# Optimization experiments

Measured on AMD Instinct MI355X. Metric: run time of the kernel, lower is better.

The kernel has to match this reference:

```python
import jax, jax.numpy as jnp
import numpy as np

B, C, Q, D = 64, 512, 64, 256  # D = 2 * hidden_size; similarity weight has 3*D = 768 entries


def _length_mask(key, batch, seqlen):
    # realistic padding masks: each row has a random valid prefix length in [seqlen//2, seqlen]
    lens = jax.random.randint(key, (batch,), seqlen // 2, seqlen + 1)
    return (jnp.arange(seqlen)[None, :] < lens[:, None]).astype(jnp.int32)


def setup_inputs() -> dict:
    key = jax.random.key(0)
    k1, k2, k3, k4, k5 = jax.random.split(key, 5)
    context = jax.random.normal(k1, (B, C, D), dtype=jnp.float32)
    question = jax.random.normal(k2, (B, Q, D), dtype=jnp.float32)
    context_mask = _length_mask(k3, B, C)
    question_mask = _length_mask(k4, B, Q)
    w = jax.random.normal(k5, (3 * D,), dtype=jnp.float32) * (1.0 / np.sqrt(3 * D))
    return {"context": context, "question": question,
            "context_mask": context_mask, "question_mask": question_mask, "w": w}


def reference(context, question, context_mask, question_mask, w):
    d = context.shape[-1]
    # Linear([c, q, c*q]) with no bias decomposes exactly into three terms.
    w_c, w_q, w_m = w[:d], w[d:2 * d], w[2 * d:]
    sim = ((context @ w_c)[:, :, None]                      # [B, C, 1]
           + (question @ w_q)[:, None, :]                   # [B, 1, Q]
           + jnp.einsum('bcd,bqd->bcq', context * w_m, question))  # [B, C, Q]
    neg = jnp.finfo(sim.dtype).min
    # context-to-query attention (mask question positions)
    sim_q = jnp.where(question_mask[:, None, :] != 0, sim, neg)
    a = jax.nn.softmax(sim_q, axis=2)                        # [B, C, Q]
    c2q = jnp.einsum('bcq,bqd->bcd', a, question)            # [B, C, D]
    # query-to-context attention (max over Q, mask context positions)
    sim_max = jnp.max(sim, axis=2)                           # [B, C]
    sim_max = jnp.where(context_mask != 0, sim_max, neg)
    b = jax.nn.softmax(sim_max, axis=1)                      # [B, C]
    q2c = jnp.einsum('bc,bcd->bd', b, context)[:, None, :]   # [B, 1, D]
    q2c = jnp.broadcast_to(q2c, context.shape)               # [B, C, D]
    g = jnp.concatenate([context, c2q, context * c2q, context * q2c], axis=-1)
    return g
```

## Files before the change

### kernel.cpp

```cpp
#include <hip/hip_runtime.h>
#include <hip/hip_bf16.h>
#include <float.h>

#define B_ 64
#define C_ 512
#define Q_ 64
#define D_ 256

typedef _Float16 f16x8 __attribute__((ext_vector_type(8)));
typedef float f32x4 __attribute__((ext_vector_type(4)));

union U4H8 { uint4 u; f16x8 h; };
union UH2 { _Float16 h[2]; uint32_t u; };

__device__ __forceinline__ uint32_t packh2(float a, float b) {
  UH2 v; v.h[0] = (_Float16)a; v.h[1] = (_Float16)b; return v.u;
}

__device__ __forceinline__ float wred_sum(float v) {
#pragma unroll
  for (int off = 32; off > 0; off >>= 1) v += __shfl_xor(v, off, 64);
  return v;
}
__device__ __forceinline__ float wred_max(float v) {
#pragma unroll
  for (int off = 32; off > 0; off >>= 1) v = fmaxf(v, __shfl_xor(v, off, 64));
  return v;
}

__global__ __launch_bounds__(256) void k_rowdot(const float* __restrict__ src,
                                                const float* __restrict__ wgt,
                                                float* __restrict__ out, int nrows) {
  int wv = threadIdx.x >> 6, ln = threadIdx.x & 63;
  int row = blockIdx.x * 4 + wv;
  if (row >= nrows) return;
  float4 s4 = *(const float4*)(src + (size_t)row * D_ + 4 * ln);
  float4 w4 = *(const float4*)(wgt + 4 * ln);
  float p = s4.x * w4.x + s4.y * w4.y + s4.z * w4.z + s4.w * w4.w;
  p = wred_sum(p);
  if (ln == 0) out[row] = p;
}

__global__ __launch_bounds__(256) void k_prepack(const float* __restrict__ qst,
                                                 const float* __restrict__ w,
                                                 uint32_t* __restrict__ qraw_img,
                                                 uint32_t* __restrict__ qT_img,
                                                 float* __restrict__ qwq) {
  const int b = blockIdx.x;
  const int sub = blockIdx.y;
  const int t = threadIdx.x;
  const float* qb = qst + (size_t)b * Q_ * D_;
#pragma unroll
  for (int it = 0; it < 8; ++it) {
    int idx = sub * 2048 + it * 256 + t;
    int q = idx >> 7, jp = idx & 127;
    float2 v = *(const float2*)(qb + q * D_ + 2 * jp);
    int ch = jp >> 2;
    int phys = (ch & ~7) | ((ch & 7) ^ (q & 7));
    qraw_img[(size_t)b * 8192 + q * 128 + phys * 4 + (jp & 3)] = packh2(v.x, v.y);
  }
  {
    int d = sub * 64 + (t >> 2);
    uint32_t* dst = qT_img + (size_t)b * 8192 + d * 32;
#pragma unroll
    for (int k = 0; k < 2; ++k) {
      int qc = (t & 3) * 2 + k;
      uint32_t tmp[4];
#pragma unroll
      for (int e = 0; e < 4; ++e) {
        int q0 = qc * 8 + e * 2;
        tmp[e] = packh2(qb[q0 * D_ + d], qb[(q0 + 1) * D_ + d]);
      }
      int pc = qc ^ (d & 7);
      *(uint4*)(dst + pc * 4) = uint4{tmp[0], tmp[1], tmp[2], tmp[3]};
    }
  }
  if (sub == 0) {
    int q = t >> 2, sl = t & 3;
    float p = 0.f;
#pragma unroll
    for (int i = 0; i < 16; ++i) {
      float4 v = *(const float4*)(qb + q * D_ + sl * 64 + i * 4);
      float4 ww = *(const float4*)(w + D_ + sl * 64 + i * 4);
      p += v.x * ww.x + v.y * ww.y + v.z * ww.z + v.w * ww.w;
    }
    p += __shfl_xor(p, 1, 64);
    p += __shfl_xor(p, 2, 64);
    if (sl == 0) qwq[b * Q_ + q] = p;
  }
}

template<int IMG>
__global__ __launch_bounds__(256, 2) void k_main(
    const float* __restrict__ ctx, const float* __restrict__ qst,
    const int* __restrict__ qmask, const float* __restrict__ w,
    const float* __restrict__ qwq_g,
    const uint32_t* __restrict__ qraw_img, const uint32_t* __restrict__ qT_img,
    float* __restrict__ g, float* __restrict__ simmax_g) {
  __shared__ __align__(16) ushort qraw[Q_ * D_];
  __shared__ __align__(16) ushort qT[D_ * Q_];
  __shared__ __align__(16) ushort pbuf[4][16 * Q_];
  __shared__ float qwq_l[Q_];
  __shared__ int   qml_l[Q_];

  const int bid = blockIdx.x;
  const int b = bid & 63;
  const int c0 = (bid >> 6) * 64;
  const int t = threadIdx.x;
  const int wv = t >> 6, ln = t & 63;
  const int lc = ln & 15;
  const int lg = ln >> 4;
  const int c0w = c0 + wv * 16;

  if constexpr (IMG) {
    const uint32_t* qr_src = qraw_img + (size_t)b * 8192;
    const uint32_t* qt_src = qT_img + (size_t)b * 8192;
#pragma unroll
    for (int i = 0; i < 8; ++i)
      __builtin_amdgcn_global_load_lds(
          (const __attribute__((address_space(1))) uint32_t*)(qr_src + i * 1024 + t * 4),
          (__attribute__((address_space(3))) uint32_t*)((uint32_t*)qraw + i * 1024 + t * 4),
          16, 0, 0);
#pragma unroll
    for (int i = 0; i < 8; ++i)
      __builtin_amdgcn_global_load_lds(
          (const __attribute__((address_space(1))) uint32_t*)(qt_src + i * 1024 + t * 4),
          (__attribute__((address_space(3))) uint32_t*)((uint32_t*)qT + i * 1024 + t * 4),
          16, 0, 0);
  }

  f16x8 bfrag[8];
  float cwc_p = 0.f;
  const float* crow = ctx + ((size_t)b * C_ + c0w + lc) * D_;
  float* grow0 = g + ((size_t)b * C_ + c0w + lc) * (4 * D_);
#pragma unroll
  for (int kk = 0; kk < 8; ++kk) {
    int kb = kk * 32 + lg * 8;
    float4 cv0 = *(const float4*)(crow + kb);
    float4 cv1 = *(const float4*)(crow + kb + 4);
    float4 wc0 = *(const float4*)(w + kb);
    float4 wc1 = *(const float4*)(w + kb + 4);
    float4 wm0 = *(const float4*)(w + 2 * D_ + kb);
    float4 wm1 = *(const float4*)(w + 2 * D_ + kb + 4);
    cwc_p += cv0.x * wc0.x + cv0.y * wc0.y + cv0.z * wc0.z + cv0.w * wc0.w
           + cv1.x * wc1.x + cv1.y * wc1.y + cv1.z * wc1.z + cv1.w * wc1.w;
    bfrag[kk][0] = (_Float16)(cv0.x * wm0.x);
    bfrag[kk][1] = (_Float16)(cv0.y * wm0.y);
    bfrag[kk][2] = (_Float16)(cv0.z * wm0.z);
    bfrag[kk][3] = (_Float16)(cv0.w * wm0.w);
    bfrag[kk][4] = (_Float16)(cv1.x * wm1.x);
    bfrag[kk][5] = (_Float16)(cv1.y * wm1.y);
    bfrag[kk][6] = (_Float16)(cv1.z * wm1.z);
    bfrag[kk][7] = (_Float16)(cv1.w * wm1.w);
    *(float4*)(grow0 + kb) = cv0;
    *(float4*)(grow0 + kb + 4) = cv1;
  }
  float cwc = cwc_p;
  cwc += __shfl_xor(cwc, 16, 64);
  cwc += __shfl_xor(cwc, 32, 64);

  if constexpr (!IMG) {
    const float* qb = qst + (size_t)b * Q_ * D_;
#pragma unroll 4
    for (int it = 0; it < 32; ++it) {
      int idx = it * 256 + t;
      int q = idx >> 7, jp = idx & 127;
      float2 v = *(const float2*)(qb + q * D_ + 2 * jp);
      int ch = jp >> 2;
      int phys = (ch & ~7) | ((ch & 7) ^ (q & 7));
      *(uint32_t*)((char*)qraw + q * 512 + phys * 16 + (jp & 3) * 4) = packh2(v.x, v.y);
    }
#pragma unroll 4
    for (int it = 0; it < 32; ++it) {
      int q = t & 63;
      int jp = (t >> 6) + 4 * it;
      float2 v = *(const float2*)(qb + q * D_ + 2 * jp);
      int d0 = 2 * jp, d1 = d0 + 1;
      UH2 h0; h0.h[0] = (_Float16)v.x;
      UH2 h1; h1.h[0] = (_Float16)v.y;
      *(ushort*)((char*)qT + d0 * 128 + (((q >> 3) ^ (d0 & 7)) << 4) + (q & 7) * 2) = (ushort)(h0.u & 0xffff);
      *(ushort*)((char*)qT + d1 * 128 + (((q >> 3) ^ (d1 & 7)) << 4) + (q & 7) * 2) = (ushort)(h1.u & 0xffff);
    }
  }
  if (t < Q_) { qwq_l[t] = qwq_g[b * Q_ + t]; qml_l[t] = qmask[b * Q_ + t]; }
  __syncthreads();

  f32x4 sacc[4];
#pragma unroll
  for (int tq = 0; tq < 4; ++tq) sacc[tq] = f32x4{0.f, 0.f, 0.f, 0.f};
#pragma unroll
  for (int tq = 0; tq < 4; ++tq) {
    int q = 16 * tq + lc;
#pragma unroll
    for (int kk = 0; kk < 8; ++kk) {
      int ch = lg + 4 * kk;
      int phys = (ch & ~7) | ((ch & 7) ^ (q & 7));
      U4H8 a; a.u = *(const uint4*)((const char*)qraw + q * 512 + phys * 16);
      sacc[tq] = __builtin_amdgcn_mfma_f32_16x16x32_f16(a.h, bfrag[kk], sacc[tq], 0, 0, 0);
    }
  }

  float vals[4][4];
  float rmax = -FLT_MAX;
#pragma unroll
  for (int tq = 0; tq < 4; ++tq) {
    float4 qw4 = *(const float4*)(qwq_l + 16 * tq + 4 * lg);
#pragma unroll
    for (int r = 0; r < 4; ++r) {
      float qv = (r == 0) ? qw4.x : (r == 1) ? qw4.y : (r == 2) ? qw4.z : qw4.w;
      vals[tq][r] = sacc[tq][r] + cwc + qv;
      rmax = fmaxf(rmax, vals[tq][r]);
    }
  }
  rmax = fmaxf(rmax, __shfl_xor(rmax, 16, 64));
  rmax = fmaxf(rmax, __shfl_xor(rmax, 32, 64));
  if (ln < 16) simmax_g[b * C_ + c0w + lc] = rmax;

  float mmax = -FLT_MAX;
#pragma unroll
  for (int tq = 0; tq < 4; ++tq) {
    int4 qm4 = *(const int4*)(qml_l + 16 * tq + 4 * lg);
#pragma unroll
    for (int r = 0; r < 4; ++r) {
      int m = (r == 0) ? qm4.x : (r == 1) ? qm4.y : (r == 2) ? qm4.z : qm4.w;
      vals[tq][r] = m ? vals[tq][r] : -FLT_MAX;
      mmax = fmaxf(mmax, vals[tq][r]);
    }
  }
  mmax = fmaxf(mmax, __shfl_xor(mmax, 16, 64));
  mmax = fmaxf(mmax, __shfl_xor(mmax, 32, 64));
  float esum = 0.f;
#pragma unroll
  for (int tq = 0; tq < 4; ++tq)
#pragma unroll
    for (int r = 0; r < 4; ++r) {
      vals[tq][r] = __expf(vals[tq][r] - mmax);
      esum += vals[tq][r];
    }
  esum += __shfl_xor(esum, 16, 64);
  esum += __shfl_xor(esum, 32, 64);
  float inv = 1.f / esum;
#pragma unroll
  for (int tq = 0; tq < 4; ++tq) {
    uint32_t p01 = packh2(vals[tq][0] * inv, vals[tq][1] * inv);
    uint32_t p23 = packh2(vals[tq][2] * inv, vals[tq][3] * inv);
    int qb4 = 16 * tq + 4 * lg;
    int phys = ((qb4 >> 3) ^ (lc & 7));
    char* dst = (char*)pbuf[wv] + lc * 128 + phys * 16 + (qb4 & 7) * 2;
    *(uint2*)dst = uint2{p01, p23};
  }

  f16x8 pfragB[2];
#pragma unroll
  for (int ks = 0; ks < 2; ++ks) {
    int phys = (lg + 4 * ks) ^ (lc & 7);
    U4H8 a; a.u = *(const uint4*)((const char*)pbuf[wv] + lc * 128 + phys * 16);
    pfragB[ks] = a.h;
  }
  const float* crow2 = ctx + ((size_t)b * C_ + c0w + lc) * D_;
  float* grow = g + ((size_t)b * C_ + c0w + lc) * (4 * D_);
#pragma unroll 4
  for (int dt = 0; dt < 16; ++dt) {
    f32x4 acc = f32x4{0.f, 0.f, 0.f, 0.f};
#pragma unroll
    for (int ks = 0; ks < 2; ++ks) {
      int d = dt * 16 + lc;
      int phys = (lg + 4 * ks) ^ (d & 7);
      U4H8 aq; aq.u = *(const uint4*)((const char*)qT + d * 128 + phys * 16);
      acc = __builtin_amdgcn_mfma_f32_16x16x32_f16(aq.h, pfragB[ks], acc, 0, 0, 0);
    }
    int dcol = dt * 16 + 4 * lg;
    float4 cvv = *(const float4*)(crow2 + dcol);
    float4 c2qv{acc[0], acc[1], acc[2], acc[3]};
    *(float4*)(grow + D_ + dcol) = c2qv;
    float4 p2{cvv.x * c2qv.x, cvv.y * c2qv.y, cvv.z * c2qv.z, cvv.w * c2qv.w};
    *(float4*)(grow + 2 * D_ + dcol) = p2;
  }
}

__global__ __launch_bounds__(256) void k_q2c_bs(const float* __restrict__ ctx,
                                                const float* __restrict__ simmax,
                                                const int* __restrict__ cmask,
                                                float* __restrict__ part) {
  int b = blockIdx.x, ch = blockIdx.y, t = threadIdx.x;
  int wv = t >> 6, ln = t & 63;
  __shared__ float bls[C_];
  __shared__ float sred[4];
  __shared__ float ssum[4];
  float v0 = simmax[b * C_ + t], v1 = simmax[b * C_ + 256 + t];
  if (!cmask[b * C_ + t]) v0 = -FLT_MAX;
  if (!cmask[b * C_ + 256 + t]) v1 = -FLT_MAX;
  float mx = wred_max(fmaxf(v0, v1));
  if (ln == 0) sred[wv] = mx;
  __syncthreads();
  float bm = fmaxf(fmaxf(sred[0], sred[1]), fmaxf(sred[2], sred[3]));
  float e0 = __expf(v0 - bm), e1 = __expf(v1 - bm);
  float ps = wred_sum(e0 + e1);
  if (ln == 0) ssum[wv] = ps;
  __syncthreads();
  float bs = ssum[0] + ssum[1] + ssum[2] + ssum[3];
  float invbs = 1.f / bs;
  bls[t] = e0 * invbs;
  bls[256 + t] = e1 * invbs;
  __syncthreads();
  float acc = 0.f;
  int cbeg = ch * 64;
#pragma unroll 4
  for (int c = cbeg; c < cbeg + 64; ++c)
    acc += bls[c] * ctx[((size_t)b * C_ + c) * D_ + t];
  part[((size_t)b * 8 + ch) * D_ + t] = acc;
}

__global__ __launch_bounds__(256) void k_g3q(const float* __restrict__ ctx,
                                             const float* __restrict__ part,
                                             float* __restrict__ g) {
  int b = blockIdx.x, ch = blockIdx.y, t = threadIdx.x;
  __shared__ float q2c_l[D_];
  float s = 0.f;
#pragma unroll
  for (int k = 0; k < 8; ++k) s += part[((size_t)b * 8 + k) * D_ + t];
  q2c_l[t] = s;
  __syncthreads();
  int d4 = t & 63;
  int ro = t >> 6;
  float4 qv = *(const float4*)(q2c_l + 4 * d4);
#pragma unroll 4
  for (int it = 0; it < 16; ++it) {
    int c = ch * 64 + it * 4 + ro;
    float4 cv = *(const float4*)(ctx + ((size_t)b * C_ + c) * D_ + 4 * d4);
    float4 o{cv.x * qv.x, cv.y * qv.y, cv.z * qv.z, cv.w * qv.w};
    *(float4*)(g + ((size_t)b * C_ + c) * (4 * D_) + 3 * D_ + 4 * d4) = o;
  }
}

extern "C" void kernel_launch(void* const* d_in, const int* in_sizes, int n_in,
                              void* d_out, int out_size, void* d_ws, size_t ws_size,
                              hipStream_t stream) {
  const float* ctx   = (const float*)d_in[0];
  const float* qst   = (const float*)d_in[1];
  const int*   cmask = (const int*)d_in[2];
  const int*   qmask = (const int*)d_in[3];
  const float* w     = (const float*)d_in[4];
  float* g  = (float*)d_out;
  float* ws = (float*)d_ws;

  float*    qwq      = ws;
  float*    simmax   = ws + 4096;
  float*    part     = ws + 36864;
  uint32_t* qraw_img = (uint32_t*)(ws + 167936);
  uint32_t* qT_img   = (uint32_t*)(ws + 692224);
  const size_t need_bytes = (size_t)(692224 + 524288) * 4;

  if (ws_size >= need_bytes) {
    k_prepack<<<dim3(B_, 4), 256, 0, stream>>>(qst, w, qraw_img, qT_img, qwq);
    k_main<1><<<dim3(512), 256, 0, stream>>>(ctx, qst, qmask, w, qwq,
                                             qraw_img, qT_img, g, simmax);
  } else {
    k_rowdot<<<dim3(B_ * Q_ / 4), 256, 0, stream>>>(qst, w + D_, qwq, B_ * Q_);
    k_main<0><<<dim3(512), 256, 0, stream>>>(ctx, qst, qmask, w, qwq,
                                             qraw_img, qT_img, g, simmax);
  }
  k_q2c_bs<<<dim3(B_, 8), 256, 0, stream>>>(ctx, simmax, cmask, part);
  k_g3q<<<dim3(B_, 8), 256, 0, stream>>>(ctx, part, g);
}
```

Baseline: 61.54 us.

## Split main kernel into sim and c2q passes, fuse q2c output writes

```diff
diff --git a/kernel.cpp b/kernel.cpp
--- a/kernel.cpp
+++ b/kernel.cpp
@@ -90,16 +90,12 @@
   }
 }
 
-template<int IMG>
-__global__ __launch_bounds__(256, 2) void k_main(
-    const float* __restrict__ ctx, const float* __restrict__ qst,
-    const int* __restrict__ qmask, const float* __restrict__ w,
-    const float* __restrict__ qwq_g,
-    const uint32_t* __restrict__ qraw_img, const uint32_t* __restrict__ qT_img,
-    float* __restrict__ g, float* __restrict__ simmax_g) {
+__global__ __launch_bounds__(256, 4) void k_sim(
+    const float* __restrict__ ctx, const int* __restrict__ qmask,
+    const float* __restrict__ w, const float* __restrict__ qwq_g,
+    const uint32_t* __restrict__ qraw_img,
+    ushort* __restrict__ P_img, float* __restrict__ simmax_g) {
   __shared__ __align__(16) ushort qraw[Q_ * D_];
-  __shared__ __align__(16) ushort qT[D_ * Q_];
-  __shared__ __align__(16) ushort pbuf[4][16 * Q_];
   __shared__ float qwq_l[Q_];
   __shared__ int   qml_l[Q_];
 
@@ -112,15 +108,129 @@
   const int lg = ln >> 4;
   const int c0w = c0 + wv * 16;
 
-  if constexpr (IMG) {
+  {
     const uint32_t* qr_src = qraw_img + (size_t)b * 8192;
-    const uint32_t* qt_src = qT_img + (size_t)b * 8192;
 #pragma unroll
     for (int i = 0; i < 8; ++i)
       __builtin_amdgcn_global_load_lds(
           (const __attribute__((address_space(1))) uint32_t*)(qr_src + i * 1024 + t * 4),
           (__attribute__((address_space(3))) uint32_t*)((uint32_t*)qraw + i * 1024 + t * 4),
           16, 0, 0);
+  }
+
+  f16x8 bfrag[8];
+  float cwc_p = 0.f;
+  const float* crow = ctx + ((size_t)b * C_ + c0w + lc) * D_;
+#pragma unroll
+  for (int kk = 0; kk < 8; ++kk) {
+    int kb = kk * 32 + lg * 8;
+    float4 cv0 = *(const float4*)(crow + kb);
+    float4 cv1 = *(const float4*)(crow + kb + 4);
+    float4 wc0 = *(const float4*)(w + kb);
+    float4 wc1 = *(const float4*)(w + kb + 4);
+    float4 wm0 = *(const float4*)(w + 2 * D_ + kb);
+    float4 wm1 = *(const float4*)(w + 2 * D_ + kb + 4);
+    cwc_p += cv0.x * wc0.x + cv0.y * wc0.y + cv0.z * wc0.z + cv0.w * wc0.w
+           + cv1.x * wc1.x + cv1.y * wc1.y + cv1.z * wc1.z + cv1.w * wc1.w;
+    bfrag[kk][0] = (_Float16)(cv0.x * wm0.x);
+    bfrag[kk][1] = (_Float16)(cv0.y * wm0.y);
+    bfrag[kk][2] = (_Float16)(cv0.z * wm0.z);
+    bfrag[kk][3] = (_Float16)(cv0.w * wm0.w);
+    bfrag[kk][4] = (_Float16)(cv1.x * wm1.x);
+    bfrag[kk][5] = (_Float16)(cv1.y * wm1.y);
+    bfrag[kk][6] = (_Float16)(cv1.z * wm1.z);
+    bfrag[kk][7] = (_Float16)(cv1.w * wm1.w);
+  }
+  float cwc = cwc_p;
+  cwc += __shfl_xor(cwc, 16, 64);
+  cwc += __shfl_xor(cwc, 32, 64);
+
+  if (t < Q_) { qwq_l[t] = qwq_g[b * Q_ + t]; qml_l[t] = qmask[b * Q_ + t]; }
+  __syncthreads();
+
+  f32x4 sacc[4];
+#pragma unroll
+  for (int tq = 0; tq < 4; ++tq) sacc[tq] = f32x4{0.f, 0.f, 0.f, 0.f};
+#pragma unroll
+  for (int tq = 0; tq < 4; ++tq) {
+    int q = 16 * tq + lc;
+#pragma unroll
+    for (int kk = 0; kk < 8; ++kk) {
+      int ch = lg + 4 * kk;
+      int phys = (ch & ~7) | ((ch & 7) ^ (q & 7));
+      U4H8 a; a.u = *(const uint4*)((const char*)qraw + q * 512 + phys * 16);
+      sacc[tq] = __builtin_amdgcn_mfma_f32_16x16x32_f16(a.h, bfrag[kk], sacc[tq], 0, 0, 0);
+    }
+  }
+
+  float vals[4][4];
+  float rmax = -FLT_MAX;
+#pragma unroll
+  for (int tq = 0; tq < 4; ++tq) {
+    float4 qw4 = *(const float4*)(qwq_l + 16 * tq + 4 * lg);
+#pragma unroll
+    for (int r = 0; r < 4; ++r) {
+      float qv = (r == 0) ? qw4.x : (r == 1) ? qw4.y : (r == 2) ? qw4.z : qw4.w;
+      vals[tq][r] = sacc[tq][r] + cwc + qv;
+      rmax = fmaxf(rmax, vals[tq][r]);
+    }
+  }
+  rmax = fmaxf(rmax, __shfl_xor(rmax, 16, 64));
+  rmax = fmaxf(rmax, __shfl_xor(rmax, 32, 64));
+  if (ln < 16) simmax_g[b * C_ + c0w + lc] = rmax;
+
+  float mmax = -FLT_MAX;
+#pragma unroll
+  for (int tq = 0; tq < 4; ++tq) {
+    int4 qm4 = *(const int4*)(qml_l + 16 * tq + 4 * lg);
+#pragma unroll
+    for (int r = 0; r < 4; ++r) {
+      int m = (r == 0) ? qm4.x : (r == 1) ? qm4.y : (r == 2) ? qm4.z : qm4.w;
+      vals[tq][r] = m ? vals[tq][r] : -FLT_MAX;
+      mmax = fmaxf(mmax, vals[tq][r]);
+    }
+  }
+  mmax = fmaxf(mmax, __shfl_xor(mmax, 16, 64));
+  mmax = fmaxf(mmax, __shfl_xor(mmax, 32, 64));
+  float esum = 0.f;
+#pragma unroll
+  for (int tq = 0; tq < 4; ++tq)
+#pragma unroll
+    for (int r = 0; r < 4; ++r) {
+      vals[tq][r] = __expf(vals[tq][r] - mmax);
+      esum += vals[tq][r];
+    }
+  esum += __shfl_xor(esum, 16, 64);
+  esum += __shfl_xor(esum, 32, 64);
+  float inv = 1.f / esum;
+  char* pdst = (char*)(P_img + ((size_t)bid * 4 + wv) * 1024);
+#pragma unroll
+  for (int tq = 0; tq < 4; ++tq) {
+    uint32_t p01 = packh2(vals[tq][0] * inv, vals[tq][1] * inv);
+    uint32_t p23 = packh2(vals[tq][2] * inv, vals[tq][3] * inv);
+    int qb4 = 16 * tq + 4 * lg;
+    *(uint2*)(pdst + lc * 128 + qb4 * 2) = uint2{p01, p23};
+  }
+}
+
+__global__ __launch_bounds__(256, 4) void k_c2q(
+    const float* __restrict__ ctx, const uint32_t* __restrict__ qT_img,
+    const ushort* __restrict__ P_img, const float* __restrict__ part,
+    float* __restrict__ g) {
+  __shared__ __align__(16) ushort qT[D_ * Q_];
+  __shared__ float q2c_l[D_];
+
+  const int bid = blockIdx.x;
+  const int b = bid & 63;
+  const int c0 = (bid >> 6) * 64;
+  const int t = threadIdx.x;
+  const int wv = t >> 6, ln = t & 63;
+  const int lc = ln & 15;
+  const int lg = ln >> 4;
+  const int c0w = c0 + wv * 16;
+
+  {
+    const uint32_t* qt_src = qT_img + (size_t)b * 8192;
 #pragma unroll
     for (int i = 0; i < 8; ++i)
       __builtin_amdgcn_global_load_lds(
@@ -128,6 +238,98 @@
           (__attribute__((address_space(3))) uint32_t*)((uint32_t*)qT + i * 1024 + t * 4),
           16, 0, 0);
   }
+  const char* psrc = (const char*)(P_img + ((size_t)bid * 4 + wv) * 1024);
+  U4H8 pf0, pf1;
+  pf0.u = *(const uint4*)(psrc + lc * 128 + lg * 16);
+  pf1.u = *(const uint4*)(psrc + lc * 128 + lg * 16 + 64);
+  {
+    float s = 0.f;
+#pragma unroll
+    for (int k = 0; k < 8; ++k) s += part[((size_t)b * 8 + k) * D_ + t];
+    q2c_l[t] = s;
+  }
+  __syncthreads();
+
+  const float* crow2 = ctx + ((size_t)b * C_ + c0w + lc) * D_;
+  float* grow = g + ((size_t)b * C_ + c0w + lc) * (4 * D_);
+#pragma unroll 4
+  for (int dt = 0; dt < 16; ++dt) {
+    f32x4 acc = f32x4{0.f, 0.f, 0.f, 0.f};
+    {
+      int d = dt * 16 + lc;
+      int phys0 = lg ^ (d & 7);
+      int phys1 = (lg + 4) ^ (d & 7);
+      U4H8 aq0; aq0.u = *(const uint4*)((const char*)qT + d * 128 + phys0 * 16);
+      U4H8 aq1; aq1.u = *(const uint4*)((const char*)qT + d * 128 + phys1 * 16);
+      acc = __builtin_amdgcn_mfma_f32_16x16x32_f16(aq0.h, pf0.h, acc, 0, 0, 0);
+      acc = __builtin_amdgcn_mfma_f32_16x16x32_f16(aq1.h, pf1.h, acc, 0, 0, 0);
+    }
+    int dcol = dt * 16 + 4 * lg;
+    float4 cvv = *(const float4*)(crow2 + dcol);
+    float4 q4 = *(const float4*)(q2c_l + dcol);
+    *(float4*)(grow + dcol) = cvv;
+    float4 c2qv{acc[0], acc[1], acc[2], acc[3]};
+    *(float4*)(grow + D_ + dcol) = c2qv;
+    float4 p2{cvv.x * c2qv.x, cvv.y * c2qv.y, cvv.z * c2qv.z, cvv.w * c2qv.w};
+    *(float4*)(grow + 2 * D_ + dcol) = p2;
+    float4 p3{cvv.x * q4.x, cvv.y * q4.y, cvv.z * q4.z, cvv.w * q4.w};
+    *(float4*)(grow + 3 * D_ + dcol) = p3;
+  }
+}
+
+__global__ __launch_bounds__(256) void k_q2c_bs(const float* __restrict__ ctx,
+                                                const float* __restrict__ simmax,
+                                                const int* __restrict__ cmask,
+                                                float* __restrict__ part) {
+  int b = blockIdx.x, ch = blockIdx.y, t = threadIdx.x;
+  int wv = t >> 6, ln = t & 63;
+  __shared__ float bls[C_];
+  __shared__ float sred[4];
+  __shared__ float ssum[4];
+  float v0 = simmax[b * C_ + t], v1 = simmax[b * C_ + 256 + t];
+  if (!cmask[b * C_ + t]) v0 = -FLT_MAX;
+  if (!cmask[b * C_ + 256 + t]) v1 = -FLT_MAX;
+  float mx = wred_max(fmaxf(v0, v1));
+  if (ln == 0) sred[wv] = mx;
+  __syncthreads();
+  float bm = fmaxf(fmaxf(sred[0], sred[1]), fmaxf(sred[2], sred[3]));
+  float e0 = __expf(v0 - bm), e1 = __expf(v1 - bm);
+  float ps = wred_sum(e0 + e1);
+  if (ln == 0) ssum[wv] = ps;
+  __syncthreads();
+  float bs = ssum[0] + ssum[1] + ssum[2] + ssum[3];
+  float invbs = 1.f / bs;
+  bls[t] = e0 * invbs;
+  bls[256 + t] = e1 * invbs;
+  __syncthreads();
+  float acc = 0.f;
+  int cbeg = ch * 64;
+#pragma unroll 4
+  for (int c = cbeg; c < cbeg + 64; ++c)
+    acc += bls[c] * ctx[((size_t)b * C_ + c) * D_ + t];
+  part[((size_t)b * 8 + ch) * D_ + t] = acc;
+}
+
+__global__ __launch_bounds__(256, 2) void k_main_fb(
+    const float* __restrict__ ctx, const float* __restrict__ qst,
+    const int* __restrict__ qmask, const float* __restrict__ w,
+    const float* __restrict__ qwq_g, float* __restrict__ g,
+    float* __restrict__ simmax_g) {
+  __shared__ __align__(16) ushort qraw[Q_ * D_];
+  __shared__ __align__(16) ushort qT[D_ * Q_];
+  __shared__ __align__(16) ushort pbuf[4][16 * Q_];
+  __shared__ float qwq_l[Q_];
+  __shared__ int   qml_l[Q_];
+
+  const int bid = blockIdx.x;
+  const int b = bid & 63;
+  const int c0 = (bid >> 6) * 64;
+  const int t = threadIdx.x;
+  const int wv = t >> 6, ln = t & 63;
+  const int lc = ln & 15;
+  const int lg = ln >> 4;
+  const int c0w = c0 + wv * 16;
+  const float* qb = qst + (size_t)b * Q_ * D_;
 
   f16x8 bfrag[8];
   float cwc_p = 0.f;
@@ -159,28 +361,25 @@
   cwc += __shfl_xor(cwc, 16, 64);
   cwc += __shfl_xor(cwc, 32, 64);
 
-  if constexpr (!IMG) {
-    const float* qb = qst + (size_t)b * Q_ * D_;
 #pragma unroll 4
-    for (int it = 0; it < 32; ++it) {
-      int idx = it * 256 + t;
-      int q = idx >> 7, jp = idx & 127;
-      float2 v = *(const float2*)(qb + q * D_ + 2 * jp);
-      int ch = jp >> 2;
-      int phys = (ch & ~7) | ((ch & 7) ^ (q & 7));
-      *(uint32_t*)((char*)qraw + q * 512 + phys * 16 + (jp & 3) * 4) = packh2(v.x, v.y);
-    }
+  for (int it = 0; it < 32; ++it) {
+    int idx = it * 256 + t;
+    int q = idx >> 7, jp = idx & 127;
+    float2 v = *(const float2*)(qb + q * D_ + 2 * jp);
+    int ch = jp >> 2;
+    int phys = (ch & ~7) | ((ch & 7) ^ (q & 7));
+    *(uint32_t*)((char*)qraw + q * 512 + phys * 16 + (jp & 3) * 4) = packh2(v.x, v.y);
+  }
 #pragma unroll 4
-    for (int it = 0; it < 32; ++it) {
-      int q = t & 63;
-      int jp = (t >> 6) + 4 * it;
-      float2 v = *(const float2*)(qb + q * D_ + 2 * jp);
-      int d0 = 2 * jp, d1 = d0 + 1;
-      UH2 h0; h0.h[0] = (_Float16)v.x;
-      UH2 h1; h1.h[0] = (_Float16)v.y;
-      *(ushort*)((char*)qT + d0 * 128 + (((q >> 3) ^ (d0 & 7)) << 4) + (q & 7) * 2) = (ushort)(h0.u & 0xffff);
-      *(ushort*)((char*)qT + d1 * 128 + (((q >> 3) ^ (d1 & 7)) << 4) + (q & 7) * 2) = (ushort)(h1.u & 0xffff);
-    }
+  for (int it = 0; it < 32; ++it) {
+    int q = t & 63;
+    int jp = (t >> 6) + 4 * it;
+    float2 v = *(const float2*)(qb + q * D_ + 2 * jp);
+    int d0 = 2 * jp, d1 = d0 + 1;
+    UH2 h0; h0.h[0] = (_Float16)v.x;
+    UH2 h1; h1.h[0] = (_Float16)v.y;
+    *(ushort*)((char*)qT + d0 * 128 + (((q >> 3) ^ (d0 & 7)) << 4) + (q & 7) * 2) = (ushort)(h0.u & 0xffff);
+    *(ushort*)((char*)qT + d1 * 128 + (((q >> 3) ^ (d1 & 7)) << 4) + (q & 7) * 2) = (ushort)(h1.u & 0xffff);
   }
   if (t < Q_) { qwq_l[t] = qwq_g[b * Q_ + t]; qml_l[t] = qmask[b * Q_ + t]; }
   __syncthreads();
@@ -199,7 +398,6 @@
       sacc[tq] = __builtin_amdgcn_mfma_f32_16x16x32_f16(a.h, bfrag[kk], sacc[tq], 0, 0, 0);
     }
   }
-
   float vals[4][4];
   float rmax = -FLT_MAX;
 #pragma unroll
@@ -215,7 +413,6 @@
   rmax = fmaxf(rmax, __shfl_xor(rmax, 16, 64));
   rmax = fmaxf(rmax, __shfl_xor(rmax, 32, 64));
   if (ln < 16) simmax_g[b * C_ + c0w + lc] = rmax;
-
   float mmax = -FLT_MAX;
 #pragma unroll
   for (int tq = 0; tq < 4; ++tq) {
@@ -249,7 +446,6 @@
     char* dst = (char*)pbuf[wv] + lc * 128 + phys * 16 + (qb4 & 7) * 2;
     *(uint2*)dst = uint2{p01, p23};
   }
-
   f16x8 pfragB[2];
 #pragma unroll
   for (int ks = 0; ks < 2; ++ks) {
@@ -276,39 +472,6 @@
     float4 p2{cvv.x * c2qv.x, cvv.y * c2qv.y, cvv.z * c2qv.z, cvv.w * c2qv.w};
     *(float4*)(grow + 2 * D_ + dcol) = p2;
   }
-}
-
-__global__ __launch_bounds__(256) void k_q2c_bs(const float* __restrict__ ctx,
-                                                const float* __restrict__ simmax,
-                                                const int* __restrict__ cmask,
-                                                float* __restrict__ part) {
-  int b = blockIdx.x, ch = blockIdx.y, t = threadIdx.x;
-  int wv = t >> 6, ln = t & 63;
-  __shared__ float bls[C_];
-  __shared__ float sred[4];
-  __shared__ float ssum[4];
-  float v0 = simmax[b * C_ + t], v1 = simmax[b * C_ + 256 + t];
-  if (!cmask[b * C_ + t]) v0 = -FLT_MAX;
-  if (!cmask[b * C_ + 256 + t]) v1 = -FLT_MAX;
-  float mx = wred_max(fmaxf(v0, v1));
-  if (ln == 0) sred[wv] = mx;
-  __syncthreads();
-  float bm = fmaxf(fmaxf(sred[0], sred[1]), fmaxf(sred[2], sred[3]));
-  float e0 = __expf(v0 - bm), e1 = __expf(v1 - bm);
-  float ps = wred_sum(e0 + e1);
-  if (ln == 0) ssum[wv] = ps;
-  __syncthreads();
-  float bs = ssum[0] + ssum[1] + ssum[2] + ssum[3];
-  float invbs = 1.f / bs;
-  bls[t] = e0 * invbs;
-  bls[256 + t] = e1 * invbs;
-  __syncthreads();
-  float acc = 0.f;
-  int cbeg = ch * 64;
-#pragma unroll 4
-  for (int c = cbeg; c < cbeg + 64; ++c)
-    acc += bls[c] * ctx[((size_t)b * C_ + c) * D_ + t];
-  part[((size_t)b * 8 + ch) * D_ + t] = acc;
 }
 
 __global__ __launch_bounds__(256) void k_g3q(const float* __restrict__ ctx,
@@ -349,17 +512,19 @@
   float*    part     = ws + 36864;
   uint32_t* qraw_img = (uint32_t*)(ws + 167936);
   uint32_t* qT_img   = (uint32_t*)(ws + 692224);
-  const size_t need_bytes = (size_t)(692224 + 524288) * 4;
+  ushort*   P_img    = (ushort*)(ws + 1216512);
+  const size_t need_bytes = (size_t)(1216512 + 1048576) * 4;
 
   if (ws_size >= need_bytes) {
     k_prepack<<<dim3(B_, 4), 256, 0, stream>>>(qst, w, qraw_img, qT_img, qwq);
-    k_main<1><<<dim3(512), 256, 0, stream>>>(ctx, qst, qmask, w, qwq,
-                                             qraw_img, qT_img, g, simmax);
+    k_sim<<<dim3(512), 256, 0, stream>>>(ctx, qmask, w, qwq, qraw_img,
+                                         P_img, simmax);
+    k_q2c_bs<<<dim3(B_, 8), 256, 0, stream>>>(ctx, simmax, cmask, part);
+    k_c2q<<<dim3(512), 256, 0, stream>>>(ctx, qT_img, P_img, part, g);
   } else {
     k_rowdot<<<dim3(B_ * Q_ / 4), 256, 0, stream>>>(qst, w + D_, qwq, B_ * Q_);
-    k_main<0><<<dim3(512), 256, 0, stream>>>(ctx, qst, qmask, w, qwq,
-                                             qraw_img, qT_img, g, simmax);
-  }
-  k_q2c_bs<<<dim3(B_, 8), 256, 0, stream>>>(ctx, simmax, cmask, part);
-  k_g3q<<<dim3(B_, 8), 256, 0, stream>>>(ctx, part, g);
-}
+    k_main_fb<<<dim3(512), 256, 0, stream>>>(ctx, qst, qmask, w, qwq, g, simmax);
+    k_q2c_bs<<<dim3(B_, 8), 256, 0, stream>>>(ctx, simmax, cmask, part);
+    k_g3q<<<dim3(B_, 8), 256, 0, stream>>>(ctx, part, g);
+  }
+}
```

New measurement: 60.68 us. Within noise of the previous version (-1.4%).
